# Performance work log

Measured on AMD Instinct MI355X. Metric: run time of the kernel, lower is better.

The kernel has to match this reference:

```python
import jax, jax.numpy as jnp
import numpy as np

E = 8          # number of routed experts
TOP_K = 2      # experts per token
D = 2048       # hidden size
DFF = 1408     # per-expert intermediate
DFF_S = 2816   # shared-expert intermediate (2 shared experts fused)
B, S = 2, 2048


def setup_inputs() -> dict:
    key = jax.random.key(0)
    ks = jax.random.split(key, 8)
    sc = 0.02
    return {
        "hidden_states": jax.random.normal(ks[0], (B, S, D), jnp.float32),
        "gate_weight": jax.random.normal(ks[1], (E, D), jnp.float32) * sc,
        "w_gate": jax.random.normal(ks[2], (E, DFF, D), jnp.float32) * sc,
        "w_up": jax.random.normal(ks[3], (E, DFF, D), jnp.float32) * sc,
        "w_down": jax.random.normal(ks[4], (E, D, DFF), jnp.float32) * sc,
        "w_shared_gate": jax.random.normal(ks[5], (DFF_S, D), jnp.float32) * sc,
        "w_shared_up": jax.random.normal(ks[6], (DFF_S, D), jnp.float32) * sc,
        "w_shared_down": jax.random.normal(ks[7], (D, DFF_S), jnp.float32) * sc,
    }


def reference(hidden_states, gate_weight, w_gate, w_up, w_down,
              w_shared_gate, w_shared_up, w_shared_down):
    orig_shape = hidden_states.shape
    x = hidden_states.reshape(-1, orig_shape[-1])      # [T, D]

    # --- router (computed under no_grad in the original) ---
    logits = x @ gate_weight.T                          # [T, E]
    scores = jax.nn.softmax(logits, axis=-1)
    topk_w, topk_idx = jax.lax.top_k(scores, TOP_K)     # [T, K]
    topk_w = topk_w / jnp.sum(topk_w, axis=-1, keepdims=True)
    topk_w = jax.lax.stop_gradient(topk_w)
    topk_idx = jax.lax.stop_gradient(topk_idx)

    # dense combine weights [T, E] (equivalent to the masked per-expert loop +
    # weighted sum over the top-k copies)
    combine = jnp.einsum('tk,tke->te', topk_w,
                         jax.nn.one_hot(topk_idx, E, dtype=x.dtype))

    # --- routed experts: SwiGLU MLP per expert, dense over E ---
    g = jnp.einsum('td,efd->etf', x, w_gate)            # [E, T, DFF]
    u = jnp.einsum('td,efd->etf', x, w_up)
    h = jax.nn.silu(g) * u
    expert_out = jnp.einsum('etf,edf->etd', h, w_down)  # [E, T, D]
    y = jnp.einsum('etd,te->td', expert_out, combine)   # [T, D]

    # --- shared experts on the identity ---
    sh = jax.nn.silu(x @ w_shared_gate.T) * (x @ w_shared_up.T)
    y = y + sh @ w_shared_down.T

    return y.reshape(orig_shape)
```

## Files before the change

### kernel.cpp

```cpp
#include <hip/hip_runtime.h>
#include <stdint.h>
#include <stdio.h>

#define T_TOK 4096
#define DMODEL 2048
#define NEXP 8
#define DFF 1408
#define DFFS 2816
#define NSLOT 8192

#define GU_GRID (16 * 22 + 39 * 11)
#define DN_GRID (16 * 8 + 39 * 8)

typedef unsigned short u16;
typedef short s16x8 __attribute__((ext_vector_type(8)));
typedef unsigned short u16x4 __attribute__((ext_vector_type(4)));
typedef __bf16 bf16x8 __attribute__((ext_vector_type(8)));
typedef float f32x4 __attribute__((ext_vector_type(4)));

__device__ __forceinline__ u16 f2bf(float f) {
  uint32_t u = __builtin_bit_cast(uint32_t, f);
  u += 0x7fffu + ((u >> 16) & 1u);
  return (u16)(u >> 16);
}
__device__ __forceinline__ float bf2f(u16 h) {
  uint32_t u = ((uint32_t)h) << 16;
  return __builtin_bit_cast(float, u);
}

__device__ __forceinline__ void gl16(const u16* g, u16* l) {
  __builtin_amdgcn_global_load_lds((const __attribute__((address_space(1))) void*)g,
                                   (__attribute__((address_space(3))) void*)l,
                                   16, 0, 0);
}

#define BARRIER() asm volatile("s_barrier" ::: "memory")

__global__ void k_convert6(const float* __restrict__ s0, u16* __restrict__ d0, int n0,
                           const float* __restrict__ s1, u16* __restrict__ d1, int n1,
                           const float* __restrict__ s2, u16* __restrict__ d2, int n2,
                           const float* __restrict__ s3, u16* __restrict__ d3, int n3,
                           const float* __restrict__ s4, u16* __restrict__ d4, int n4,
                           const float* __restrict__ s5, u16* __restrict__ d5, int n5) {
  int total = n0 + n1 + n2 + n3 + n4 + n5;
  int stride = gridDim.x * 256;
  for (int i = blockIdx.x * 256 + threadIdx.x; i < total; i += stride) {
    const float* s; u16* d; int k = i;
    if (k < n0) { s = s0; d = d0; }
    else { k -= n0;
      if (k < n1) { s = s1; d = d1; }
      else { k -= n1;
        if (k < n2) { s = s2; d = d2; }
        else { k -= n2;
          if (k < n3) { s = s3; d = d3; }
          else { k -= n3;
            if (k < n4) { s = s4; d = d4; }
            else { k -= n4; s = s5; d = d5; }
          }
        }
      }
    }
    float4 a = ((const float4*)s)[2 * k];
    float4 b = ((const float4*)s)[2 * k + 1];
    s16x8 r;
    r[0] = (short)f2bf(a.x); r[1] = (short)f2bf(a.y);
    r[2] = (short)f2bf(a.z); r[3] = (short)f2bf(a.w);
    r[4] = (short)f2bf(b.x); r[5] = (short)f2bf(b.y);
    r[6] = (short)f2bf(b.z); r[7] = (short)f2bf(b.w);
    ((s16x8*)d)[k] = r;
  }
}

__global__ void k_zero(int* __restrict__ counts) {
  if (threadIdx.x < NEXP) counts[threadIdx.x] = 0;
}

__global__ void k_router(const float* __restrict__ x, const float* __restrict__ gw,
                         u16* __restrict__ xb,
                         float* __restrict__ tkw, int* __restrict__ tki,
                         int* __restrict__ counts) {
  __shared__ double sm[NEXP];
  int t = blockIdx.x;
  int tid = threadIdx.x;
  int lane = tid & 63, wv = tid >> 6;
  const float4* xr = (const float4*)(x + (size_t)t * DMODEL);
  const float4* gr = (const float4*)gw;
  int e0 = wv * 2, e1 = e0 + 1;
  double a0 = 0.0, a1 = 0.0;
#pragma unroll
  for (int it = 0; it < DMODEL / 4 / 64; ++it) {
    int idx = it * 64 + lane;
    float4 xv = xr[idx];
    float4 g0 = gr[e0 * (DMODEL / 4) + idx];
    float4 g1 = gr[e1 * (DMODEL / 4) + idx];
    a0 += (double)xv.x * g0.x + (double)xv.y * g0.y +
          (double)xv.z * g0.z + (double)xv.w * g0.w;
    a1 += (double)xv.x * g1.x + (double)xv.y * g1.y +
          (double)xv.z * g1.z + (double)xv.w * g1.w;
    if (wv == 0) {
      u16x4 r = { f2bf(xv.x), f2bf(xv.y), f2bf(xv.z), f2bf(xv.w) };
      ((u16x4*)(xb + (size_t)t * DMODEL))[idx] = r;
    }
  }
#pragma unroll
  for (int off = 32; off; off >>= 1) {
    a0 += __shfl_down(a0, off, 64);
    a1 += __shfl_down(a1, off, 64);
  }
  if (lane == 0) { sm[e0] = a0; sm[e1] = a1; }
  __syncthreads();
  if (tid == 0) {
    double acc[NEXP];
#pragma unroll
    for (int e = 0; e < NEXP; ++e) acc[e] = sm[e];
    int i0 = 0; double v0 = acc[0];
    for (int e = 1; e < NEXP; ++e) if (acc[e] > v0) { v0 = acc[e]; i0 = e; }
    int i1 = -1; double v1 = -1e300;
    for (int e = 0; e < NEXP; ++e) if (e != i0 && acc[e] > v1) { v1 = acc[e]; i1 = e; }
    double r = exp(v1 - v0);
    float w0 = (float)(1.0 / (1.0 + r));
    float w1 = 1.0f - w0;
    tkw[2 * t] = w0; tkw[2 * t + 1] = w1;
    tki[2 * t] = i0; tki[2 * t + 1] = i1;
    atomicAdd(&counts[i0], 1);
    atomicAdd(&counts[i1], 1);
  }
}

__global__ void k_scan_sched(const int* __restrict__ counts, int* __restrict__ offs,
                             int* __restrict__ cursor, int* __restrict__ tblGU,
                             int* __restrict__ tblDN, int* __restrict__ nact) {
  if (threadIdx.x != 0 || blockIdx.x != 0) return;
  int s = 0;
  for (int e = 0; e < NEXP; ++e) { offs[e] = s; cursor[e] = s; s += counts[e]; }
  offs[NEXP] = s;
  int g = 0, d = 0;
  for (int m = 0; m < T_TOK / 256; ++m) {
    for (int nb = 0; nb < DFFS * 2 / 256; ++nb)
      tblGU[g++] = (int)(0x80000000u | (m << 12) | nb);
    for (int nb = 0; nb < DMODEL / 256; ++nb)
      tblDN[d++] = (int)(0x80000000u | (m << 12) | nb);
  }
  for (int e = 0; e < NEXP; ++e) {
    int mb = (counts[e] + 255) >> 8;
    for (int m = 0; m < mb; ++m) {
      for (int nb = 0; nb < DFF * 2 / 256; ++nb)
        tblGU[g++] = (e << 24) | (m << 12) | nb;
      for (int nb = 0; nb < DMODEL / 256; ++nb)
        tblDN[d++] = (e << 24) | (m << 12) | nb;
    }
  }
  nact[0] = g; nact[1] = d;
}

__global__ void k_assign(const int* __restrict__ tki, int* __restrict__ cursor,
                         int* __restrict__ pos, int* __restrict__ slot_tok) {
  int t = blockIdx.x * 256 + threadIdx.x;
  if (t >= T_TOK) return;
#pragma unroll
  for (int k = 0; k < 2; ++k) {
    int e = tki[2 * t + k];
    int p = atomicAdd(&cursor[e], 1);
    pos[2 * t + k] = p;
    slot_tok[p] = t;
  }
}

template <int PHASE>
__launch_bounds__(512, 2)
__global__ void k_gemm8(const int* __restrict__ tbl, const int* __restrict__ nact,
                        const u16* __restrict__ xb,
                        const u16* __restrict__ hr, const u16* __restrict__ hs,
                        const u16* __restrict__ wbg, const u16* __restrict__ wbu,
                        const u16* __restrict__ wbd,
                        const u16* __restrict__ wbsg, const u16* __restrict__ wbsu,
                        const u16* __restrict__ wbsd,
                        u16* __restrict__ P1r, u16* __restrict__ P2r,
                        u16* __restrict__ P1s, u16* __restrict__ P2s,
                        u16* __restrict__ yr, float* __restrict__ out,
                        const int* __restrict__ offs, const int* __restrict__ counts,
                        const int* __restrict__ slot_tok) {
  __shared__ __attribute__((aligned(16))) u16 lds[2 * 32768];

  if ((int)blockIdx.x >= nact[PHASE]) return;
  const int desc = tbl[blockIdx.x];
  const bool shrd = desc < 0;
  const int e = (desc >> 24) & 0xF;
  const int m0 = ((desc >> 12) & 0xFFF) * 256;
  const int n0 = (desc & 0xFFF) * 256;

  const u16 *A, *B1, *B2;
  u16 *C1, *C2;
  float* OF = nullptr;
  int base, cnt, nsplit, K;
  bool gather = false;
  if constexpr (PHASE == 0) {
    K = DMODEL;
    if (shrd) {
      A = xb; base = 0; cnt = T_TOK;
      B1 = wbsg; B2 = wbsu; C1 = P1s; C2 = P2s; nsplit = DFFS;
    } else {
      A = xb; gather = true; base = offs[e]; cnt = counts[e];
      size_t es = (size_t)e * DFF * DMODEL;
      B1 = wbg + es; B2 = wbu + es; C1 = P1r; C2 = P2r; nsplit = DFF;
    }
  } else {
    nsplit = DMODEL;
    if (shrd) {
      A = hs; base = 0; cnt = T_TOK; K = DFFS;
      B1 = B2 = wbsd; OF = out; C1 = C2 = nullptr;
    } else {
      A = hr; base = offs[e]; cnt = counts[e]; K = DFF;
      B1 = B2 = wbd + (size_t)e * DMODEL * DFF; C1 = C2 = yr;
    }
  }
  const int NT = K >> 6;

  int tid = threadIdx.x;
  int lane = tid & 63, wv = tid >> 6;
  int wm = wv >> 2, wn = wv & 3;
  int fr = lane & 15, fq = lane >> 4;

  int srow = tid >> 3;
  int sslot = (tid & 7) ^ (srow & 7);
  const u16* ap[4]; const u16* bp[4];
#pragma unroll
  for (int h = 0; h < 4; ++h) {
    int r = h * 64 + srow;
    int ra = m0 + r; ra = ra < cnt ? ra : cnt - 1;
    int ga = gather ? slot_tok[base + ra] : base + ra;
    ap[h] = A + (size_t)ga * K + sslot * 8;
    int nc = n0 + r;
    const u16* bb = (nc >= nsplit) ? (B2 + (size_t)(nc - nsplit) * K)
                                   : (B1 + (size_t)nc * K);
    bp[h] = bb + sslot * 8;
  }

#define STG_A(h, bufi, kt) gl16(ap[h] + (size_t)(kt) * 64, \
                                lds + (bufi) * 32768 + (h) * 4096 + wv * 512)
#define STG_B(h, bufi, kt) gl16(bp[h] + (size_t)(kt) * 64, \
                                lds + (bufi) * 32768 + 16384 + (h) * 4096 + wv * 512)

  int sKs0 = ((0 + fq) ^ (fr & 7)) * 8;
  int sKs1 = ((4 + fq) ^ (fr & 7)) * 8;
  int aBase = wm * 8192 + fr * 64;
  int bBase = 16384 + (wn >> 1) * 8192 + ((wn & 1) * 64 + fr) * 64;

  f32x4 acc[8][4];
#pragma unroll
  for (int i = 0; i < 8; ++i)
#pragma unroll
    for (int j = 0; j < 4; ++j) acc[i][j] = (f32x4){0.f, 0.f, 0.f, 0.f};

  STG_A(0, 0, 0); STG_A(1, 0, 0); STG_A(2, 0, 0); STG_A(3, 0, 0);
  STG_B(0, 0, 0); STG_B(1, 0, 0); STG_B(2, 0, 0); STG_B(3, 0, 0);
  if (NT > 1) { STG_A(0, 1, 1); STG_A(1, 1, 1); STG_A(2, 1, 1); STG_A(3, 1, 1); }
  if (NT > 1) asm volatile("s_waitcnt vmcnt(4)" ::: "memory");
  else        asm volatile("s_waitcnt vmcnt(0)" ::: "memory");
  BARRIER();
  __builtin_amdgcn_sched_barrier(0);

  bf16x8 rAa[4][2], rAb[4][2], rB01[2][2], rB23[2][2];
#pragma unroll
  for (int il = 0; il < 4; ++il) {
    rAa[il][0] = *(const bf16x8*)(lds + aBase + il * 1024 + sKs0);
    rAa[il][1] = *(const bf16x8*)(lds + aBase + il * 1024 + sKs1);
  }
#pragma unroll
  for (int jl = 0; jl < 2; ++jl) {
    rB01[jl][0] = *(const bf16x8*)(lds + bBase + jl * 1024 + sKs0);
    rB01[jl][1] = *(const bf16x8*)(lds + bBase + jl * 1024 + sKs1);
  }

  for (int t = 0; t < NT; ++t) {
    const int buf = t & 1, nbuf = buf ^ 1;
    const u16* lbuf = lds + buf * 32768;
    const u16* lbufN = lds + nbuf * 32768;
    const bool hn1 = (t + 1) < NT, hn2 = (t + 2) < NT;

#pragma unroll
    for (int jl = 0; jl < 2; ++jl) {
      rB23[jl][0] = *(const bf16x8*)(lbuf + bBase + (2 + jl) * 1024 + sKs0);
      rB23[jl][1] = *(const bf16x8*)(lbuf + bBase + (2 + jl) * 1024 + sKs1);
    }
    if (hn1) { STG_B(0, nbuf, t + 1); STG_B(1, nbuf, t + 1); }
    __builtin_amdgcn_s_setprio(1);
#pragma unroll
    for (int il = 0; il < 4; ++il)
#pragma unroll
      for (int jl = 0; jl < 2; ++jl) {
        acc[il][jl] = __builtin_amdgcn_mfma_f32_16x16x32_bf16(rAa[il][0], rB01[jl][0], acc[il][jl], 0, 0, 0);
        acc[il][jl] = __builtin_amdgcn_mfma_f32_16x16x32_bf16(rAa[il][1], rB01[jl][1], acc[il][jl], 0, 0, 0);
      }
    __builtin_amdgcn_s_setprio(0);

#pragma unroll
    for (int il = 0; il < 4; ++il) {
      rAb[il][0] = *(const bf16x8*)(lbuf + aBase + (4 + il) * 1024 + sKs0);
      rAb[il][1] = *(const bf16x8*)(lbuf + aBase + (4 + il) * 1024 + sKs1);
    }
    if (hn1) { STG_B(2, nbuf, t + 1); STG_B(3, nbuf, t + 1); }
    __builtin_amdgcn_s_setprio(1);
#pragma unroll
    for (int il = 0; il < 4; ++il)
#pragma unroll
      for (int jl = 0; jl < 2; ++jl) {
        acc[il][2 + jl] = __builtin_amdgcn_mfma_f32_16x16x32_bf16(rAa[il][0], rB23[jl][0], acc[il][2 + jl], 0, 0, 0);
        acc[il][2 + jl] = __builtin_amdgcn_mfma_f32_16x16x32_bf16(rAa[il][1], rB23[jl][1], acc[il][2 + jl], 0, 0, 0);
      }
    __builtin_amdgcn_s_setprio(0);

    asm volatile("s_waitcnt lgkmcnt(0)" ::: "memory");
    BARRIER();
    __builtin_amdgcn_sched_barrier(0);
    if (hn2) { STG_A(0, buf, t + 2); STG_A(1, buf, t + 2); }
    __builtin_amdgcn_s_setprio(1);
#pragma unroll
    for (int il = 0; il < 4; ++il)
#pragma unroll
      for (int jl = 0; jl < 2; ++jl) {
        acc[4 + il][jl] = __builtin_amdgcn_mfma_f32_16x16x32_bf16(rAb[il][0], rB01[jl][0], acc[4 + il][jl], 0, 0, 0);
        acc[4 + il][jl] = __builtin_amdgcn_mfma_f32_16x16x32_bf16(rAb[il][1], rB01[jl][1], acc[4 + il][jl], 0, 0, 0);
      }
    __builtin_amdgcn_s_setprio(0);

    if (hn1) {
      if (hn2) asm volatile("s_waitcnt vmcnt(2)" ::: "memory");
      else     asm volatile("s_waitcnt vmcnt(0)" ::: "memory");
      BARRIER();
      __builtin_amdgcn_sched_barrier(0);
      if (hn2) { STG_A(2, buf, t + 2); STG_A(3, buf, t + 2); }
#pragma unroll
      for (int il = 0; il < 4; ++il) {
        rAa[il][0] = *(const bf16x8*)(lbufN + aBase + il * 1024 + sKs0);
        rAa[il][1] = *(const bf16x8*)(lbufN + aBase + il * 1024 + sKs1);
      }
#pragma unroll
      for (int jl = 0; jl < 2; ++jl) {
        rB01[jl][0] = *(const bf16x8*)(lbufN + bBase + jl * 1024 + sKs0);
        rB01[jl][1] = *(const bf16x8*)(lbufN + bBase + jl * 1024 + sKs1);
      }
    }
    __builtin_amdgcn_s_setprio(1);
#pragma unroll
    for (int il = 0; il < 4; ++il)
#pragma unroll
      for (int jl = 0; jl < 2; ++jl) {
        acc[4 + il][2 + jl] = __builtin_amdgcn_mfma_f32_16x16x32_bf16(rAb[il][0], rB23[jl][0], acc[4 + il][2 + jl], 0, 0, 0);
        acc[4 + il][2 + jl] = __builtin_amdgcn_mfma_f32_16x16x32_bf16(rAb[il][1], rB23[jl][1], acc[4 + il][2 + jl], 0, 0, 0);
      }
    __builtin_amdgcn_s_setprio(0);
  }
#undef STG_A
#undef STG_B

#pragma unroll
  for (int i = 0; i < 8; ++i) {
    int row_t = wm * 128 + i * 16 + fq * 4;
#pragma unroll
    for (int r = 0; r < 4; ++r) {
      int m = m0 + row_t + r;
      if (m >= cnt) continue;
      size_t rowoff = (size_t)(base + m) * (size_t)nsplit;
#pragma unroll
      for (int j = 0; j < 4; ++j) {
        int col_t = n0 + wn * 64 + j * 16 + fr;
        float v = acc[i][j][r];
        if (PHASE == 1 && shrd)      OF[rowoff + col_t] = v;
        else if (col_t >= nsplit)    C2[rowoff + col_t - nsplit] = f2bf(v);
        else                         C1[rowoff + col_t] = f2bf(v);
      }
    }
  }
}

__global__ void k_silu2(const u16* __restrict__ g1, const u16* __restrict__ u1,
                        u16* __restrict__ h1, int n1,
                        const u16* __restrict__ g2, const u16* __restrict__ u2,
                        u16* __restrict__ h2, int n2) {
  int i = blockIdx.x * 256 + threadIdx.x;
  const u16 *g, *u; u16* h; int idx;
  if (i < n1) { g = g1; u = u1; h = h1; idx = i; }
  else { idx = i - n1; if (idx >= n2) return; g = g2; u = u2; h = h2; }
  s16x8 gv = ((const s16x8*)g)[idx];
  s16x8 uv = ((const s16x8*)u)[idx];
  s16x8 hv;
#pragma unroll
  for (int j = 0; j < 8; ++j) {
    float gf = bf2f((u16)gv[j]);
    float uf = bf2f((u16)uv[j]);
    float s = gf / (1.f + __expf(-gf));
    hv[j] = (short)f2bf(s * uf);
  }
  ((s16x8*)h)[idx] = hv;
}

__global__ void k_combine(float* __restrict__ y, const u16* __restrict__ yr,
                          const float* __restrict__ tkw, const int* __restrict__ pos) {
  int t = blockIdx.x;
  int i = threadIdx.x;
  float w0 = tkw[2 * t], w1 = tkw[2 * t + 1];
  size_t p0 = (size_t)pos[2 * t] * DMODEL, p1 = (size_t)pos[2 * t + 1] * DMODEL;
  int d0 = i * 8;
  s16x8 a = *(const s16x8*)(yr + p0 + d0);
  s16x8 b = *(const s16x8*)(yr + p1 + d0);
  float* yo = y + (size_t)t * DMODEL + d0;
#pragma unroll
  for (int j = 0; j < 8; ++j)
    yo[j] += w0 * bf2f((u16)a[j]) + w1 * bf2f((u16)b[j]);
}

extern "C" void kernel_launch(void* const* d_in, const int* in_sizes, int n_in,
                              void* d_out, int out_size, void* d_ws, size_t ws_size,
                              hipStream_t stream) {
  const float* x   = (const float*)d_in[0];
  const float* gw  = (const float*)d_in[1];
  const float* wg  = (const float*)d_in[2];
  const float* wu  = (const float*)d_in[3];
  const float* wd  = (const float*)d_in[4];
  const float* wsg = (const float*)d_in[5];
  const float* wsu = (const float*)d_in[6];
  const float* wsd = (const float*)d_in[7];
  float* out = (float*)d_out;

  char* ws = (char*)d_ws;
  size_t o = 0;
  auto alloc = [&](size_t bytes) -> void* {
    void* p = ws + o;
    o += (bytes + 255) & ~(size_t)255;
    return p;
  };
  u16* xb   = (u16*)alloc((size_t)T_TOK * DMODEL * 2);
  u16* wbg  = (u16*)alloc((size_t)NEXP * DFF * DMODEL * 2);
  u16* wbu  = (u16*)alloc((size_t)NEXP * DFF * DMODEL * 2);
  u16* wbd  = (u16*)alloc((size_t)NEXP * DMODEL * DFF * 2);
  u16* wbsg = (u16*)alloc((size_t)DFFS * DMODEL * 2);
  u16* wbsu = (u16*)alloc((size_t)DFFS * DMODEL * 2);
  u16* wbsd = (u16*)alloc((size_t)DMODEL * DFFS * 2);
  u16* P1r  = (u16*)alloc((size_t)NSLOT * DFF * 2);
  u16* P1s  = (u16*)alloc((size_t)T_TOK * DFFS * 2);
  u16* P2r  = (u16*)alloc((size_t)NSLOT * DFF * 2);
  u16* P2s  = (u16*)alloc((size_t)T_TOK * DFFS * 2);
  u16* yr   = P2r;
  float* tkw = (float*)alloc((size_t)T_TOK * 2 * 4);
  int* tki   = (int*)alloc((size_t)T_TOK * 2 * 4);
  int* pos   = (int*)alloc((size_t)T_TOK * 2 * 4);
  int* slot_tok = (int*)alloc((size_t)NSLOT * 4);
  int* counts   = (int*)alloc(64);
  int* offs     = (int*)alloc(64);
  int* cursor   = (int*)alloc(64);
  int* tblGU    = (int*)alloc(GU_GRID * 4);
  int* tblDN    = (int*)alloc(DN_GRID * 4);
  int* nact     = (int*)alloc(64);
  if (o > ws_size) {
    fprintf(stderr, "kernel_launch: ws too small: need %zu have %zu\n", o, ws_size);
    return;
  }

  {
    int n8w = NEXP * DFF * DMODEL / 8;
    int n8s = DFFS * DMODEL / 8;
    k_convert6<<<2048, 256, 0, stream>>>(wg, wbg, n8w, wu, wbu, n8w, wd, wbd, n8w,
                                         wsg, wbsg, n8s, wsu, wbsu, n8s, wsd, wbsd, n8s);
  }

  k_zero<<<1, 64, 0, stream>>>(counts);
  k_router<<<T_TOK, 256, 0, stream>>>(x, gw, xb, tkw, tki, counts);
  k_scan_sched<<<1, 64, 0, stream>>>(counts, offs, cursor, tblGU, tblDN, nact);
  k_assign<<<(T_TOK + 255) / 256, 256, 0, stream>>>(tki, cursor, pos, slot_tok);

  k_gemm8<0><<<GU_GRID, 512, 0, stream>>>(
      tblGU, nact, xb, nullptr, nullptr,
      wbg, wbu, wbd, wbsg, wbsu, wbsd,
      P1r, P2r, P1s, P2s, yr, out, offs, counts, slot_tok);

  {
    int n1 = NSLOT * DFF / 8, n2 = T_TOK * DFFS / 8;
    k_silu2<<<(n1 + n2 + 255) / 256, 256, 0, stream>>>(
        P1r, P2r, P1r, n1, P1s, P2s, P1s, n2);
  }

  k_gemm8<1><<<DN_GRID, 512, 0, stream>>>(
      tblDN, nact, xb, P1r, P1s,
      wbg, wbu, wbd, wbsg, wbsu, wbsd,
      P1r, P2r, P1s, P2s, yr, out, offs, counts, slot_tok);

  k_combine<<<T_TOK, 256, 0, stream>>>(out, yr, tkw, pos);
}
```

Baseline: 584.7 us.

## Fuse fp32-to-bf16 weight conversion into GEMM B-tile staging

Drops the separate weight-conversion kernel. The GEMMs now load fp32 weights into registers, convert them to bf16 and write them to LDS themselves. The main loop is also restructured: all four A slices are staged at once, and LDS fragments are reloaded per k-step instead of being prefetched across the barrier. This removes a full read and write of all weights (about 250MB of fp32), but the B path no longer uses async global-to-LDS loads. It also reads twice the bytes per tile, and weight tiles are converted once per M-tile, so the total B traffic can grow.

Result: slower. 597.9 us (+2.3%).

```diff
diff --git a/kernel.cpp b/kernel.cpp
--- a/kernel.cpp
+++ b/kernel.cpp
@@ -35,41 +35,7 @@
 }
 
 #define BARRIER() asm volatile("s_barrier" ::: "memory")
-
-__global__ void k_convert6(const float* __restrict__ s0, u16* __restrict__ d0, int n0,
-                           const float* __restrict__ s1, u16* __restrict__ d1, int n1,
-                           const float* __restrict__ s2, u16* __restrict__ d2, int n2,
-                           const float* __restrict__ s3, u16* __restrict__ d3, int n3,
-                           const float* __restrict__ s4, u16* __restrict__ d4, int n4,
-                           const float* __restrict__ s5, u16* __restrict__ d5, int n5) {
-  int total = n0 + n1 + n2 + n3 + n4 + n5;
-  int stride = gridDim.x * 256;
-  for (int i = blockIdx.x * 256 + threadIdx.x; i < total; i += stride) {
-    const float* s; u16* d; int k = i;
-    if (k < n0) { s = s0; d = d0; }
-    else { k -= n0;
-      if (k < n1) { s = s1; d = d1; }
-      else { k -= n1;
-        if (k < n2) { s = s2; d = d2; }
-        else { k -= n2;
-          if (k < n3) { s = s3; d = d3; }
-          else { k -= n3;
-            if (k < n4) { s = s4; d = d4; }
-            else { k -= n4; s = s5; d = d5; }
-          }
-        }
-      }
-    }
-    float4 a = ((const float4*)s)[2 * k];
-    float4 b = ((const float4*)s)[2 * k + 1];
-    s16x8 r;
-    r[0] = (short)f2bf(a.x); r[1] = (short)f2bf(a.y);
-    r[2] = (short)f2bf(a.z); r[3] = (short)f2bf(a.w);
-    r[4] = (short)f2bf(b.x); r[5] = (short)f2bf(b.y);
-    r[6] = (short)f2bf(b.z); r[7] = (short)f2bf(b.w);
-    ((s16x8*)d)[k] = r;
-  }
-}
+#define SBAR()    __builtin_amdgcn_sched_barrier(0)
 
 __global__ void k_zero(int* __restrict__ counts) {
   if (threadIdx.x < NEXP) counts[threadIdx.x] = 0;
@@ -171,10 +137,10 @@
 __global__ void k_gemm8(const int* __restrict__ tbl, const int* __restrict__ nact,
                         const u16* __restrict__ xb,
                         const u16* __restrict__ hr, const u16* __restrict__ hs,
-                        const u16* __restrict__ wbg, const u16* __restrict__ wbu,
-                        const u16* __restrict__ wbd,
-                        const u16* __restrict__ wbsg, const u16* __restrict__ wbsu,
-                        const u16* __restrict__ wbsd,
+                        const float* __restrict__ wgF, const float* __restrict__ wuF,
+                        const float* __restrict__ wdF,
+                        const float* __restrict__ wsgF, const float* __restrict__ wsuF,
+                        const float* __restrict__ wsdF,
                         u16* __restrict__ P1r, u16* __restrict__ P2r,
                         u16* __restrict__ P1s, u16* __restrict__ P2s,
                         u16* __restrict__ yr, float* __restrict__ out,
@@ -189,7 +155,8 @@
   const int m0 = ((desc >> 12) & 0xFFF) * 256;
   const int n0 = (desc & 0xFFF) * 256;
 
-  const u16 *A, *B1, *B2;
+  const u16* A;
+  const float *B1f, *B2f;
   u16 *C1, *C2;
   float* OF = nullptr;
   int base, cnt, nsplit, K;
@@ -198,20 +165,20 @@
     K = DMODEL;
     if (shrd) {
       A = xb; base = 0; cnt = T_TOK;
-      B1 = wbsg; B2 = wbsu; C1 = P1s; C2 = P2s; nsplit = DFFS;
+      B1f = wsgF; B2f = wsuF; C1 = P1s; C2 = P2s; nsplit = DFFS;
     } else {
       A = xb; gather = true; base = offs[e]; cnt = counts[e];
       size_t es = (size_t)e * DFF * DMODEL;
-      B1 = wbg + es; B2 = wbu + es; C1 = P1r; C2 = P2r; nsplit = DFF;
+      B1f = wgF + es; B2f = wuF + es; C1 = P1r; C2 = P2r; nsplit = DFF;
     }
   } else {
     nsplit = DMODEL;
     if (shrd) {
       A = hs; base = 0; cnt = T_TOK; K = DFFS;
-      B1 = B2 = wbsd; OF = out; C1 = C2 = nullptr;
+      B1f = B2f = wsdF; OF = out; C1 = C2 = nullptr;
     } else {
       A = hr; base = offs[e]; cnt = counts[e]; K = DFF;
-      B1 = B2 = wbd + (size_t)e * DMODEL * DFF; C1 = C2 = yr;
+      B1f = B2f = wdF + (size_t)e * DMODEL * DFF; C1 = C2 = yr;
     }
   }
   const int NT = K >> 6;
@@ -223,7 +190,7 @@
 
   int srow = tid >> 3;
   int sslot = (tid & 7) ^ (srow & 7);
-  const u16* ap[4]; const u16* bp[4];
+  const u16* ap[4]; const float* bpf[4];
 #pragma unroll
   for (int h = 0; h < 4; ++h) {
     int r = h * 64 + srow;
@@ -231,15 +198,21 @@
     int ga = gather ? slot_tok[base + ra] : base + ra;
     ap[h] = A + (size_t)ga * K + sslot * 8;
     int nc = n0 + r;
-    const u16* bb = (nc >= nsplit) ? (B2 + (size_t)(nc - nsplit) * K)
-                                   : (B1 + (size_t)nc * K);
-    bp[h] = bb + sslot * 8;
+    const float* bb = (nc >= nsplit) ? (B2f + (size_t)(nc - nsplit) * K)
+                                     : (B1f + (size_t)nc * K);
+    bpf[h] = bb + sslot * 8;
   }
 
 #define STG_A(h, bufi, kt) gl16(ap[h] + (size_t)(kt) * 64, \
                                 lds + (bufi) * 32768 + (h) * 4096 + wv * 512)
-#define STG_B(h, bufi, kt) gl16(bp[h] + (size_t)(kt) * 64, \
-                                lds + (bufi) * 32768 + 16384 + (h) * 4096 + wv * 512)
+#define LDB(h, kt) { breg[2*(h)]   = *(const float4*)(bpf[h] + (size_t)(kt) * 64); \
+                     breg[2*(h)+1] = *(const float4*)(bpf[h] + (size_t)(kt) * 64 + 4); }
+#define WRB(h, bufi) { s16x8 v_; \
+    v_[0] = (short)f2bf(breg[2*(h)].x);   v_[1] = (short)f2bf(breg[2*(h)].y); \
+    v_[2] = (short)f2bf(breg[2*(h)].z);   v_[3] = (short)f2bf(breg[2*(h)].w); \
+    v_[4] = (short)f2bf(breg[2*(h)+1].x); v_[5] = (short)f2bf(breg[2*(h)+1].y); \
+    v_[6] = (short)f2bf(breg[2*(h)+1].z); v_[7] = (short)f2bf(breg[2*(h)+1].w); \
+    *(s16x8*)(lds + (bufi) * 32768 + 16384 + (h) * 4096 + wv * 512 + lane * 8) = v_; }
 
   int sKs0 = ((0 + fq) ^ (fr & 7)) * 8;
   int sKs1 = ((4 + fq) ^ (fr & 7)) * 8;
@@ -252,107 +225,111 @@
 #pragma unroll
     for (int j = 0; j < 4; ++j) acc[i][j] = (f32x4){0.f, 0.f, 0.f, 0.f};
 
+  float4 breg[8];
+
+  LDB(0, 0); LDB(1, 0); LDB(2, 0); LDB(3, 0);
   STG_A(0, 0, 0); STG_A(1, 0, 0); STG_A(2, 0, 0); STG_A(3, 0, 0);
-  STG_B(0, 0, 0); STG_B(1, 0, 0); STG_B(2, 0, 0); STG_B(3, 0, 0);
-  if (NT > 1) { STG_A(0, 1, 1); STG_A(1, 1, 1); STG_A(2, 1, 1); STG_A(3, 1, 1); }
-  if (NT > 1) asm volatile("s_waitcnt vmcnt(4)" ::: "memory");
-  else        asm volatile("s_waitcnt vmcnt(0)" ::: "memory");
+  WRB(0, 0); WRB(1, 0); WRB(2, 0); WRB(3, 0);
+  if (NT > 1) {
+    LDB(0, 1); LDB(1, 1); LDB(2, 1); LDB(3, 1);
+    STG_A(0, 1, 1); STG_A(1, 1, 1); STG_A(2, 1, 1); STG_A(3, 1, 1);
+    asm volatile("s_waitcnt vmcnt(12)" ::: "memory");
+  } else {
+    asm volatile("s_waitcnt vmcnt(0)" ::: "memory");
+  }
+  asm volatile("s_waitcnt lgkmcnt(0)" ::: "memory");
   BARRIER();
-  __builtin_amdgcn_sched_barrier(0);
-
-  bf16x8 rAa[4][2], rAb[4][2], rB01[2][2], rB23[2][2];
-#pragma unroll
-  for (int il = 0; il < 4; ++il) {
-    rAa[il][0] = *(const bf16x8*)(lds + aBase + il * 1024 + sKs0);
-    rAa[il][1] = *(const bf16x8*)(lds + aBase + il * 1024 + sKs1);
-  }
-#pragma unroll
-  for (int jl = 0; jl < 2; ++jl) {
-    rB01[jl][0] = *(const bf16x8*)(lds + bBase + jl * 1024 + sKs0);
-    rB01[jl][1] = *(const bf16x8*)(lds + bBase + jl * 1024 + sKs1);
-  }
-
+  SBAR();
+
+  bf16x8 rA[4][2], rB01[2][2], rB23[2][2];
   for (int t = 0; t < NT; ++t) {
     const int buf = t & 1, nbuf = buf ^ 1;
     const u16* lbuf = lds + buf * 32768;
-    const u16* lbufN = lds + nbuf * 32768;
     const bool hn1 = (t + 1) < NT, hn2 = (t + 2) < NT;
+
+#pragma unroll
+    for (int il = 0; il < 4; ++il) {
+      rA[il][0] = *(const bf16x8*)(lbuf + aBase + il * 1024 + sKs0);
+      rA[il][1] = *(const bf16x8*)(lbuf + aBase + il * 1024 + sKs1);
+    }
+#pragma unroll
+    for (int jl = 0; jl < 2; ++jl) {
+      rB01[jl][0] = *(const bf16x8*)(lbuf + bBase + jl * 1024 + sKs0);
+      rB01[jl][1] = *(const bf16x8*)(lbuf + bBase + jl * 1024 + sKs1);
+    }
+    asm volatile("s_waitcnt lgkmcnt(0)" ::: "memory");
+    SBAR();
+    __builtin_amdgcn_s_setprio(1);
+#pragma unroll
+    for (int il = 0; il < 4; ++il)
+#pragma unroll
+      for (int jl = 0; jl < 2; ++jl) {
+        acc[il][jl] = __builtin_amdgcn_mfma_f32_16x16x32_bf16(rA[il][0], rB01[jl][0], acc[il][jl], 0, 0, 0);
+        acc[il][jl] = __builtin_amdgcn_mfma_f32_16x16x32_bf16(rA[il][1], rB01[jl][1], acc[il][jl], 0, 0, 0);
+      }
+    __builtin_amdgcn_s_setprio(0);
+    SBAR();
 
 #pragma unroll
     for (int jl = 0; jl < 2; ++jl) {
       rB23[jl][0] = *(const bf16x8*)(lbuf + bBase + (2 + jl) * 1024 + sKs0);
       rB23[jl][1] = *(const bf16x8*)(lbuf + bBase + (2 + jl) * 1024 + sKs1);
     }
-    if (hn1) { STG_B(0, nbuf, t + 1); STG_B(1, nbuf, t + 1); }
+    asm volatile("s_waitcnt lgkmcnt(0)" ::: "memory");
+    SBAR();
     __builtin_amdgcn_s_setprio(1);
 #pragma unroll
     for (int il = 0; il < 4; ++il)
 #pragma unroll
       for (int jl = 0; jl < 2; ++jl) {
-        acc[il][jl] = __builtin_amdgcn_mfma_f32_16x16x32_bf16(rAa[il][0], rB01[jl][0], acc[il][jl], 0, 0, 0);
-        acc[il][jl] = __builtin_amdgcn_mfma_f32_16x16x32_bf16(rAa[il][1], rB01[jl][1], acc[il][jl], 0, 0, 0);
+        acc[il][2 + jl] = __builtin_amdgcn_mfma_f32_16x16x32_bf16(rA[il][0], rB23[jl][0], acc[il][2 + jl], 0, 0, 0);
+        acc[il][2 + jl] = __builtin_amdgcn_mfma_f32_16x16x32_bf16(rA[il][1], rB23[jl][1], acc[il][2 + jl], 0, 0, 0);
       }
     __builtin_amdgcn_s_setprio(0);
+    SBAR();
 
 #pragma unroll
     for (int il = 0; il < 4; ++il) {
-      rAb[il][0] = *(const bf16x8*)(lbuf + aBase + (4 + il) * 1024 + sKs0);
-      rAb[il][1] = *(const bf16x8*)(lbuf + aBase + (4 + il) * 1024 + sKs1);
-    }
-    if (hn1) { STG_B(2, nbuf, t + 1); STG_B(3, nbuf, t + 1); }
+      rA[il][0] = *(const bf16x8*)(lbuf + aBase + (4 + il) * 1024 + sKs0);
+      rA[il][1] = *(const bf16x8*)(lbuf + aBase + (4 + il) * 1024 + sKs1);
+    }
+    if (hn1) {
+      asm volatile("s_waitcnt vmcnt(0)" ::: "memory");
+      SBAR();
+      WRB(0, nbuf); WRB(1, nbuf); WRB(2, nbuf); WRB(3, nbuf);
+      if (hn2) { LDB(0, t + 2); LDB(1, t + 2); LDB(2, t + 2); LDB(3, t + 2); }
+    }
+    asm volatile("s_waitcnt lgkmcnt(0)" ::: "memory");
+    SBAR();
     __builtin_amdgcn_s_setprio(1);
 #pragma unroll
     for (int il = 0; il < 4; ++il)
 #pragma unroll
       for (int jl = 0; jl < 2; ++jl) {
-        acc[il][2 + jl] = __builtin_amdgcn_mfma_f32_16x16x32_bf16(rAa[il][0], rB23[jl][0], acc[il][2 + jl], 0, 0, 0);
-        acc[il][2 + jl] = __builtin_amdgcn_mfma_f32_16x16x32_bf16(rAa[il][1], rB23[jl][1], acc[il][2 + jl], 0, 0, 0);
+        acc[4 + il][jl] = __builtin_amdgcn_mfma_f32_16x16x32_bf16(rA[il][0], rB01[jl][0], acc[4 + il][jl], 0, 0, 0);
+        acc[4 + il][jl] = __builtin_amdgcn_mfma_f32_16x16x32_bf16(rA[il][1], rB01[jl][1], acc[4 + il][jl], 0, 0, 0);
       }
     __builtin_amdgcn_s_setprio(0);
-
-    asm volatile("s_waitcnt lgkmcnt(0)" ::: "memory");
+    SBAR();
+
     BARRIER();
-    __builtin_amdgcn_sched_barrier(0);
-    if (hn2) { STG_A(0, buf, t + 2); STG_A(1, buf, t + 2); }
+    SBAR();
+    if (hn2) { STG_A(0, buf, t + 2); STG_A(1, buf, t + 2);
+               STG_A(2, buf, t + 2); STG_A(3, buf, t + 2); }
     __builtin_amdgcn_s_setprio(1);
 #pragma unroll
     for (int il = 0; il < 4; ++il)
 #pragma unroll
       for (int jl = 0; jl < 2; ++jl) {
-        acc[4 + il][jl] = __builtin_amdgcn_mfma_f32_16x16x32_bf16(rAb[il][0], rB01[jl][0], acc[4 + il][jl], 0, 0, 0);
-        acc[4 + il][jl] = __builtin_amdgcn_mfma_f32_16x16x32_bf16(rAb[il][1], rB01[jl][1], acc[4 + il][jl], 0, 0, 0);
+        acc[4 + il][2 + jl] = __builtin_amdgcn_mfma_f32_16x16x32_bf16(rA[il][0], rB23[jl][0], acc[4 + il][2 + jl], 0, 0, 0);
+        acc[4 + il][2 + jl] = __builtin_amdgcn_mfma_f32_16x16x32_bf16(rA[il][1], rB23[jl][1], acc[4 + il][2 + jl], 0, 0, 0);
       }
     __builtin_amdgcn_s_setprio(0);
-
-    if (hn1) {
-      if (hn2) asm volatile("s_waitcnt vmcnt(2)" ::: "memory");
-      else     asm volatile("s_waitcnt vmcnt(0)" ::: "memory");
-      BARRIER();
-      __builtin_amdgcn_sched_barrier(0);
-      if (hn2) { STG_A(2, buf, t + 2); STG_A(3, buf, t + 2); }
-#pragma unroll
-      for (int il = 0; il < 4; ++il) {
-        rAa[il][0] = *(const bf16x8*)(lbufN + aBase + il * 1024 + sKs0);
-        rAa[il][1] = *(const bf16x8*)(lbufN + aBase + il * 1024 + sKs1);
-      }
-#pragma unroll
-      for (int jl = 0; jl < 2; ++jl) {
-        rB01[jl][0] = *(const bf16x8*)(lbufN + bBase + jl * 1024 + sKs0);
-        rB01[jl][1] = *(const bf16x8*)(lbufN + bBase + jl * 1024 + sKs1);
-      }
-    }
-    __builtin_amdgcn_s_setprio(1);
-#pragma unroll
-    for (int il = 0; il < 4; ++il)
-#pragma unroll
-      for (int jl = 0; jl < 2; ++jl) {
-        acc[4 + il][2 + jl] = __builtin_amdgcn_mfma_f32_16x16x32_bf16(rAb[il][0], rB23[jl][0], acc[4 + il][2 + jl], 0, 0, 0);
-        acc[4 + il][2 + jl] = __builtin_amdgcn_mfma_f32_16x16x32_bf16(rAb[il][1], rB23[jl][1], acc[4 + il][2 + jl], 0, 0, 0);
-      }
-    __builtin_amdgcn_s_setprio(0);
+    SBAR();
   }
 #undef STG_A
-#undef STG_B
+#undef LDB
+#undef WRB
 
 #pragma unroll
   for (int i = 0; i < 8; ++i) {
@@ -431,12 +408,6 @@
     return p;
   };
   u16* xb   = (u16*)alloc((size_t)T_TOK * DMODEL * 2);
-  u16* wbg  = (u16*)alloc((size_t)NEXP * DFF * DMODEL * 2);
-  u16* wbu  = (u16*)alloc((size_t)NEXP * DFF * DMODEL * 2);
-  u16* wbd  = (u16*)alloc((size_t)NEXP * DMODEL * DFF * 2);
-  u16* wbsg = (u16*)alloc((size_t)DFFS * DMODEL * 2);
-  u16* wbsu = (u16*)alloc((size_t)DFFS * DMODEL * 2);
-  u16* wbsd = (u16*)alloc((size_t)DMODEL * DFFS * 2);
   u16* P1r  = (u16*)alloc((size_t)NSLOT * DFF * 2);
   u16* P1s  = (u16*)alloc((size_t)T_TOK * DFFS * 2);
   u16* P2r  = (u16*)alloc((size_t)NSLOT * DFF * 2);
@@ -457,13 +428,6 @@
     return;
   }
 
-  {
-    int n8w = NEXP * DFF * DMODEL / 8;
-    int n8s = DFFS * DMODEL / 8;
-    k_convert6<<<2048, 256, 0, stream>>>(wg, wbg, n8w, wu, wbu, n8w, wd, wbd, n8w,
-                                         wsg, wbsg, n8s, wsu, wbsu, n8s, wsd, wbsd, n8s);
-  }
-
   k_zero<<<1, 64, 0, stream>>>(counts);
   k_router<<<T_TOK, 256, 0, stream>>>(x, gw, xb, tkw, tki, counts);
   k_scan_sched<<<1, 64, 0, stream>>>(counts, offs, cursor, tblGU, tblDN, nact);
@@ -471,7 +435,7 @@
 
   k_gemm8<0><<<GU_GRID, 512, 0, stream>>>(
       tblGU, nact, xb, nullptr, nullptr,
-      wbg, wbu, wbd, wbsg, wbsu, wbsd,
+      wg, wu, wd, wsg, wsu, wsd,
       P1r, P2r, P1s, P2s, yr, out, offs, counts, slot_tok);
 
   {
@@ -482,7 +446,7 @@
 
   k_gemm8<1><<<DN_GRID, 512, 0, stream>>>(
       tblDN, nact, xb, P1r, P1s,
-      wbg, wbu, wbd, wbsg, wbsu, wbsd,
+      wg, wu, wd, wsg, wsu, wsd,
       P1r, P2r, P1s, P2s, yr, out, offs, counts, slot_tok);
 
   k_combine<<<T_TOK, 256, 0, stream>>>(out, yr, tkw, pos);
```

## Fuse SiLU-gating into gate/up GEMM epilogue by interleaving gate and up columns

Applied to the files above, without the earlier changes.

The gate/up GEMM tile now loads matching gate and up weight rows side by side within each warp's column group, so each thread holds both g and u accumulators for the same output column. The epilogue computes silu(g)*u directly and writes only the hidden activation, which removes the separate SiLU kernel and the round trip through the intermediate gate and up buffers. Each tile now covers 128 output columns instead of 256 split across gate and up, so the tile count stays the same. The routed output buffer gets its own allocation because it previously aliased the removed buffer.

Result: faster. 555.3 us (-5.0%).

```diff
diff --git a/kernel.cpp b/kernel.cpp
--- a/kernel.cpp
+++ b/kernel.cpp
@@ -35,6 +35,7 @@
 }
 
 #define BARRIER() asm volatile("s_barrier" ::: "memory")
+#define SBAR()    __builtin_amdgcn_sched_barrier(0)
 
 __global__ void k_convert6(const float* __restrict__ s0, u16* __restrict__ d0, int n0,
                            const float* __restrict__ s1, u16* __restrict__ d1, int n1,
@@ -136,7 +137,7 @@
   offs[NEXP] = s;
   int g = 0, d = 0;
   for (int m = 0; m < T_TOK / 256; ++m) {
-    for (int nb = 0; nb < DFFS * 2 / 256; ++nb)
+    for (int nb = 0; nb < DFFS / 128; ++nb)
       tblGU[g++] = (int)(0x80000000u | (m << 12) | nb);
     for (int nb = 0; nb < DMODEL / 256; ++nb)
       tblDN[d++] = (int)(0x80000000u | (m << 12) | nb);
@@ -144,7 +145,7 @@
   for (int e = 0; e < NEXP; ++e) {
     int mb = (counts[e] + 255) >> 8;
     for (int m = 0; m < mb; ++m) {
-      for (int nb = 0; nb < DFF * 2 / 256; ++nb)
+      for (int nb = 0; nb < DFF / 128; ++nb)
         tblGU[g++] = (e << 24) | (m << 12) | nb;
       for (int nb = 0; nb < DMODEL / 256; ++nb)
         tblDN[d++] = (e << 24) | (m << 12) | nb;
@@ -175,8 +176,7 @@
                         const u16* __restrict__ wbd,
                         const u16* __restrict__ wbsg, const u16* __restrict__ wbsu,
                         const u16* __restrict__ wbsd,
-                        u16* __restrict__ P1r, u16* __restrict__ P2r,
-                        u16* __restrict__ P1s, u16* __restrict__ P2s,
+                        u16* __restrict__ P1r, u16* __restrict__ P1s,
                         u16* __restrict__ yr, float* __restrict__ out,
                         const int* __restrict__ offs, const int* __restrict__ counts,
                         const int* __restrict__ slot_tok) {
@@ -187,31 +187,31 @@
   const bool shrd = desc < 0;
   const int e = (desc >> 24) & 0xF;
   const int m0 = ((desc >> 12) & 0xFFF) * 256;
-  const int n0 = (desc & 0xFFF) * 256;
-
-  const u16 *A, *B1, *B2;
-  u16 *C1, *C2;
+  const int n0 = (desc & 0xFFF) * (PHASE == 0 ? 128 : 256);
+
+  const u16 *A, *Bg, *Bu;
+  u16* C1;
   float* OF = nullptr;
-  int base, cnt, nsplit, K;
+  int base, cnt, HS, K;
   bool gather = false;
   if constexpr (PHASE == 0) {
     K = DMODEL;
     if (shrd) {
       A = xb; base = 0; cnt = T_TOK;
-      B1 = wbsg; B2 = wbsu; C1 = P1s; C2 = P2s; nsplit = DFFS;
+      Bg = wbsg; Bu = wbsu; C1 = P1s; HS = DFFS;
     } else {
       A = xb; gather = true; base = offs[e]; cnt = counts[e];
       size_t es = (size_t)e * DFF * DMODEL;
-      B1 = wbg + es; B2 = wbu + es; C1 = P1r; C2 = P2r; nsplit = DFF;
+      Bg = wbg + es; Bu = wbu + es; C1 = P1r; HS = DFF;
     }
   } else {
-    nsplit = DMODEL;
+    HS = DMODEL;
     if (shrd) {
       A = hs; base = 0; cnt = T_TOK; K = DFFS;
-      B1 = B2 = wbsd; OF = out; C1 = C2 = nullptr;
+      Bg = Bu = wbsd; OF = out; C1 = nullptr;
     } else {
       A = hr; base = offs[e]; cnt = counts[e]; K = DFF;
-      B1 = B2 = wbd + (size_t)e * DMODEL * DFF; C1 = C2 = yr;
+      Bg = Bu = wbd + (size_t)e * DMODEL * DFF; C1 = yr;
     }
   }
   const int NT = K >> 6;
@@ -230,9 +230,14 @@
     int ra = m0 + r; ra = ra < cnt ? ra : cnt - 1;
     int ga = gather ? slot_tok[base + ra] : base + ra;
     ap[h] = A + (size_t)ga * K + sslot * 8;
-    int nc = n0 + r;
-    const u16* bb = (nc >= nsplit) ? (B2 + (size_t)(nc - nsplit) * K)
-                                   : (B1 + (size_t)nc * K);
+    const u16* bb;
+    if constexpr (PHASE == 0) {
+      int wnr = r >> 6, s = r & 63;
+      int col = n0 + wnr * 32 + (s & 31);
+      bb = (s < 32 ? Bg : Bu) + (size_t)col * K;
+    } else {
+      bb = Bg + (size_t)(n0 + r) * K;
+    }
     bp[h] = bb + sslot * 8;
   }
 
@@ -258,7 +263,7 @@
   if (NT > 1) asm volatile("s_waitcnt vmcnt(4)" ::: "memory");
   else        asm volatile("s_waitcnt vmcnt(0)" ::: "memory");
   BARRIER();
-  __builtin_amdgcn_sched_barrier(0);
+  SBAR();
 
   bf16x8 rAa[4][2], rAb[4][2], rB01[2][2], rB23[2][2];
 #pragma unroll
@@ -312,7 +317,7 @@
 
     asm volatile("s_waitcnt lgkmcnt(0)" ::: "memory");
     BARRIER();
-    __builtin_amdgcn_sched_barrier(0);
+    SBAR();
     if (hn2) { STG_A(0, buf, t + 2); STG_A(1, buf, t + 2); }
     __builtin_amdgcn_s_setprio(1);
 #pragma unroll
@@ -328,7 +333,7 @@
       if (hn2) asm volatile("s_waitcnt vmcnt(2)" ::: "memory");
       else     asm volatile("s_waitcnt vmcnt(0)" ::: "memory");
       BARRIER();
-      __builtin_amdgcn_sched_barrier(0);
+      SBAR();
       if (hn2) { STG_A(2, buf, t + 2); STG_A(3, buf, t + 2); }
 #pragma unroll
       for (int il = 0; il < 4; ++il) {
@@ -361,38 +366,26 @@
     for (int r = 0; r < 4; ++r) {
       int m = m0 + row_t + r;
       if (m >= cnt) continue;
-      size_t rowoff = (size_t)(base + m) * (size_t)nsplit;
-#pragma unroll
-      for (int j = 0; j < 4; ++j) {
-        int col_t = n0 + wn * 64 + j * 16 + fr;
-        float v = acc[i][j][r];
-        if (PHASE == 1 && shrd)      OF[rowoff + col_t] = v;
-        else if (col_t >= nsplit)    C2[rowoff + col_t - nsplit] = f2bf(v);
-        else                         C1[rowoff + col_t] = f2bf(v);
-      }
-    }
-  }
-}
-
-__global__ void k_silu2(const u16* __restrict__ g1, const u16* __restrict__ u1,
-                        u16* __restrict__ h1, int n1,
-                        const u16* __restrict__ g2, const u16* __restrict__ u2,
-                        u16* __restrict__ h2, int n2) {
-  int i = blockIdx.x * 256 + threadIdx.x;
-  const u16 *g, *u; u16* h; int idx;
-  if (i < n1) { g = g1; u = u1; h = h1; idx = i; }
-  else { idx = i - n1; if (idx >= n2) return; g = g2; u = u2; h = h2; }
-  s16x8 gv = ((const s16x8*)g)[idx];
-  s16x8 uv = ((const s16x8*)u)[idx];
-  s16x8 hv;
-#pragma unroll
-  for (int j = 0; j < 8; ++j) {
-    float gf = bf2f((u16)gv[j]);
-    float uf = bf2f((u16)uv[j]);
-    float s = gf / (1.f + __expf(-gf));
-    hv[j] = (short)f2bf(s * uf);
-  }
-  ((s16x8*)h)[idx] = hv;
+      size_t rowoff = (size_t)(base + m) * (size_t)HS;
+      if constexpr (PHASE == 0) {
+#pragma unroll
+        for (int jl = 0; jl < 2; ++jl) {
+          float g = acc[i][jl][r];
+          float u = acc[i][2 + jl][r];
+          float hval = (g / (1.f + __expf(-g))) * u;
+          C1[rowoff + (n0 + wn * 32 + jl * 16 + fr)] = f2bf(hval);
+        }
+      } else {
+#pragma unroll
+        for (int j = 0; j < 4; ++j) {
+          int col_t = n0 + wn * 64 + j * 16 + fr;
+          float v = acc[i][j][r];
+          if (shrd) OF[rowoff + col_t] = v;
+          else      C1[rowoff + col_t] = f2bf(v);
+        }
+      }
+    }
+  }
 }
 
 __global__ void k_combine(float* __restrict__ y, const u16* __restrict__ yr,
@@ -439,9 +432,7 @@
   u16* wbsd = (u16*)alloc((size_t)DMODEL * DFFS * 2);
   u16* P1r  = (u16*)alloc((size_t)NSLOT * DFF * 2);
   u16* P1s  = (u16*)alloc((size_t)T_TOK * DFFS * 2);
-  u16* P2r  = (u16*)alloc((size_t)NSLOT * DFF * 2);
-  u16* P2s  = (u16*)alloc((size_t)T_TOK * DFFS * 2);
-  u16* yr   = P2r;
+  u16* yr   = (u16*)alloc((size_t)NSLOT * DMODEL * 2);
   float* tkw = (float*)alloc((size_t)T_TOK * 2 * 4);
   int* tki   = (int*)alloc((size_t)T_TOK * 2 * 4);
   int* pos   = (int*)alloc((size_t)T_TOK * 2 * 4);
@@ -472,18 +463,12 @@
   k_gemm8<0><<<GU_GRID, 512, 0, stream>>>(
       tblGU, nact, xb, nullptr, nullptr,
       wbg, wbu, wbd, wbsg, wbsu, wbsd,
-      P1r, P2r, P1s, P2s, yr, out, offs, counts, slot_tok);
-
-  {
-    int n1 = NSLOT * DFF / 8, n2 = T_TOK * DFFS / 8;
-    k_silu2<<<(n1 + n2 + 255) / 256, 256, 0, stream>>>(
-        P1r, P2r, P1r, n1, P1s, P2s, P1s, n2);
-  }
+      P1r, P1s, yr, out, offs, counts, slot_tok);
 
   k_gemm8<1><<<DN_GRID, 512, 0, stream>>>(
       tblDN, nact, xb, P1r, P1s,
       wbg, wbu, wbd, wbsg, wbsu, wbsd,
-      P1r, P2r, P1s, P2s, yr, out, offs, counts, slot_tok);
+      P1r, P1s, yr, out, offs, counts, slot_tok);
 
   k_combine<<<T_TOK, 256, 0, stream>>>(out, yr, tkw, pos);
 }
```
